# Optimization experiments

Hardware: AMD Instinct MI355X
Metric: run time of the kernel (lower is better)

Reference implementation:

```python
import jax, jax.numpy as jnp
import numpy as np

EPS = 1e-5  # torch LayerNorm default


def setup_inputs() -> dict:
    key = jax.random.key(0)
    ks = jax.random.split(key, 16)
    B, S, E = 2, 2048, 1024
    H, DK, DV = 16, 64, 64
    s_in = 1.0 / np.sqrt(E)
    s_ctx = 1.0 / np.sqrt(H * DV)
    return {
        "Q": jax.random.normal(ks[0], (B, S, E), jnp.float32),
        "K": jax.random.normal(ks[1], (B, S, E), jnp.float32),
        "V": jax.random.normal(ks[2], (B, S, E), jnp.float32),
        "attn_mask": jax.random.randint(ks[3], (B, S, S), 0, 2).astype(bool),
        "Wq": jax.random.normal(ks[4], (E, H * DK), jnp.float32) * s_in,
        "bq": jnp.zeros((H * DK,), jnp.float32),
        "Wk": jax.random.normal(ks[5], (E, H * DK), jnp.float32) * s_in,
        "bk": jnp.zeros((H * DK,), jnp.float32),
        "Wv": jax.random.normal(ks[6], (E, H * DV), jnp.float32) * s_in,
        "bv": jnp.zeros((H * DV,), jnp.float32),
        "Wo": jax.random.normal(ks[7], (H * DV, E), jnp.float32) * s_ctx,
        "bo": jnp.zeros((E,), jnp.float32),
        "gamma": jnp.ones((E,), jnp.float32),
        "beta": jnp.zeros((E,), jnp.float32),
        "n_heads": 16,
        "d_k": 64,
        "d_v": 64,
    }


def reference(Q, K, V, attn_mask, Wq, bq, Wk, bk, Wv, bv, Wo, bo, gamma, beta,
              n_heads, d_k, d_v):
    B, S, E = Q.shape
    # QKV projections -> [B, H, S, d]
    q = (Q @ Wq + bq).reshape(B, S, n_heads, d_k).transpose(0, 2, 1, 3)
    k = (K @ Wk + bk).reshape(B, S, n_heads, d_k).transpose(0, 2, 1, 3)
    v = (V @ Wv + bv).reshape(B, S, n_heads, d_v).transpose(0, 2, 1, 3)
    # scaled dot-product attention with explicit [B,H,S,S] scores
    scores = jnp.einsum('bhqd,bhkd->bhqk', q, k) / np.sqrt(d_k).astype(jnp.float32)
    scores = jnp.where(attn_mask[:, None, :, :], jnp.float32(-1e9), scores)
    attn = jax.nn.softmax(scores, axis=-1)
    context = jnp.einsum('bhqk,bhkd->bhqd', attn, v)
    context = context.transpose(0, 2, 1, 3).reshape(B, S, n_heads * d_v)
    output = context @ Wo + bo
    # residual + LayerNorm over last dim
    x = output + Q
    mu = jnp.mean(x, axis=-1, keepdims=True)
    var = jnp.mean(jnp.square(x - mu), axis=-1, keepdims=True)
    y = (x - mu) * jax.lax.rsqrt(var + EPS) * gamma + beta
    return (y, attn)
```

## Files before the change

### kernel.cpp

```cpp
#include <hip/hip_runtime.h>
#include <cstdint>
#include <cstddef>

#define Bc 2
#define Sc 2048
#define Ec 1024
#define Hc 16
#define Dc 64
#define BSc 4096
#define BHc 32

typedef __attribute__((ext_vector_type(8))) short bf16x8;
typedef __attribute__((ext_vector_type(4))) float f32x4;

__device__ __forceinline__ uint16_t f2b(float x) {
  union { float f; uint32_t u; } v; v.f = x;
  return (uint16_t)((v.u + 0x7FFFu + ((v.u >> 16) & 1u)) >> 16);
}

__device__ __forceinline__ uint4 pack8(const float* f) {
  union { uint16_t u[8]; uint4 v; } pk;
#pragma unroll
  for (int i = 0; i < 8; i++) pk.u[i] = f2b(f[i]);
  return pk.v;
}

__global__ void conv_bf16(const float* __restrict__ src, uint16_t* __restrict__ dst, int n) {
  int i = (blockIdx.x * blockDim.x + threadIdx.x) * 4;
  if (i < n) {
    float4 v = *(const float4*)(src + i);
    ushort4 o;
    o.x = f2b(v.x); o.y = f2b(v.y); o.z = f2b(v.z); o.w = f2b(v.w);
    *(ushort4*)(dst + i) = o;
  }
}

__global__ void transpose_bf16(const float* __restrict__ src, uint16_t* __restrict__ dst) {
  __shared__ uint16_t tile[32][33];
  int x0 = blockIdx.x * 32, y0 = blockIdx.y * 32;
  int tx = threadIdx.x & 31, ty = threadIdx.x >> 5;
#pragma unroll
  for (int i = 0; i < 32; i += 8)
    tile[ty + i][tx] = f2b(src[(size_t)(y0 + ty + i) * 1024 + x0 + tx]);
  __syncthreads();
#pragma unroll
  for (int i = 0; i < 32; i += 8)
    dst[(size_t)(x0 + ty + i) * 1024 + y0 + tx] = tile[tx][ty + i];
}

__global__ __launch_bounds__(256) void gemm_proj(
    const uint16_t* __restrict__ A, const uint16_t* __restrict__ BT,
    const float* __restrict__ bias, uint16_t* __restrict__ out, int mode) {
  const int K = 1024;
  __shared__ uint16_t As[128 * 40];
  __shared__ uint16_t Bs[128 * 40];
  int n0 = blockIdx.x * 128, m0 = blockIdx.y * 128;
  int t = threadIdx.x;
  int wave = t >> 6, lane = t & 63;
  int wm = (wave >> 1) * 64, wn = (wave & 1) * 64;
  int quad = lane >> 4, l16 = lane & 15;

  f32x4 acc[4][4];
#pragma unroll
  for (int i = 0; i < 4; i++)
#pragma unroll
    for (int j = 0; j < 4; j++) acc[i][j] = (f32x4)(0.0f);

  int srow = t >> 1, scol = (t & 1) * 16;

  for (int k0 = 0; k0 < K; k0 += 32) {
    const uint16_t* ag = A + (size_t)(m0 + srow) * K + k0 + scol;
    const uint16_t* bg = BT + (size_t)(n0 + srow) * K + k0 + scol;
    uint4 av0 = *(const uint4*)ag;
    uint4 av1 = *(const uint4*)(ag + 8);
    uint4 bv0 = *(const uint4*)bg;
    uint4 bv1 = *(const uint4*)(bg + 8);
    __syncthreads();
    *(uint4*)(As + srow * 40 + scol) = av0;
    *(uint4*)(As + srow * 40 + scol + 8) = av1;
    *(uint4*)(Bs + srow * 40 + scol) = bv0;
    *(uint4*)(Bs + srow * 40 + scol + 8) = bv1;
    __syncthreads();
    bf16x8 af[4], bfr[4];
#pragma unroll
    for (int i = 0; i < 4; i++)
      af[i] = *(const bf16x8*)(As + (wm + i * 16 + l16) * 40 + quad * 8);
#pragma unroll
    for (int j = 0; j < 4; j++)
      bfr[j] = *(const bf16x8*)(Bs + (wn + j * 16 + l16) * 40 + quad * 8);
#pragma unroll
    for (int i = 0; i < 4; i++)
#pragma unroll
      for (int j = 0; j < 4; j++)
        acc[i][j] = __builtin_amdgcn_mfma_f32_16x16x32_bf16(af[i], bfr[j], acc[i][j], 0, 0, 0);
  }
#pragma unroll
  for (int i = 0; i < 4; i++)
#pragma unroll
    for (int j = 0; j < 4; j++) {
      int col = n0 + wn + j * 16 + l16;
      float bval = bias[col];
      int h = col >> 6, d = col & 63;
#pragma unroll
      for (int r = 0; r < 4; r++) {
        int row = m0 + wm + i * 16 + quad * 4 + r;
        int b = row >> 11, s = row & 2047;
        uint16_t hv = f2b(acc[i][j][r] + bval);
        if (mode == 0)
          out[(size_t)((b * Hc + h) * Sc + s) * Dc + d] = hv;
        else
          out[(size_t)((b * Hc + h) * Dc + d) * Sc + s] = hv;
      }
    }
}

__global__ __launch_bounds__(256) void gemm_out(
    const uint16_t* __restrict__ A, const uint16_t* __restrict__ BT,
    const float* __restrict__ bias, const float* __restrict__ resid,
    float* __restrict__ x) {
  const int K = 1024;
  __shared__ uint16_t As[128 * 40];
  __shared__ uint16_t Bs[128 * 40];
  int n0 = blockIdx.x * 128, m0 = blockIdx.y * 128;
  int t = threadIdx.x;
  int wave = t >> 6, lane = t & 63;
  int wm = (wave >> 1) * 64, wn = (wave & 1) * 64;
  int quad = lane >> 4, l16 = lane & 15;

  f32x4 acc[4][4];
#pragma unroll
  for (int i = 0; i < 4; i++)
#pragma unroll
    for (int j = 0; j < 4; j++) acc[i][j] = (f32x4)(0.0f);

  int srow = t >> 1, scol = (t & 1) * 16;
  for (int k0 = 0; k0 < K; k0 += 32) {
    const uint16_t* ag = A + (size_t)(m0 + srow) * K + k0 + scol;
    const uint16_t* bg = BT + (size_t)(n0 + srow) * K + k0 + scol;
    uint4 av0 = *(const uint4*)ag;
    uint4 av1 = *(const uint4*)(ag + 8);
    uint4 bv0 = *(const uint4*)bg;
    uint4 bv1 = *(const uint4*)(bg + 8);
    __syncthreads();
    *(uint4*)(As + srow * 40 + scol) = av0;
    *(uint4*)(As + srow * 40 + scol + 8) = av1;
    *(uint4*)(Bs + srow * 40 + scol) = bv0;
    *(uint4*)(Bs + srow * 40 + scol + 8) = bv1;
    __syncthreads();
    bf16x8 af[4], bfr[4];
#pragma unroll
    for (int i = 0; i < 4; i++)
      af[i] = *(const bf16x8*)(As + (wm + i * 16 + l16) * 40 + quad * 8);
#pragma unroll
    for (int j = 0; j < 4; j++)
      bfr[j] = *(const bf16x8*)(Bs + (wn + j * 16 + l16) * 40 + quad * 8);
#pragma unroll
    for (int i = 0; i < 4; i++)
#pragma unroll
      for (int j = 0; j < 4; j++)
        acc[i][j] = __builtin_amdgcn_mfma_f32_16x16x32_bf16(af[i], bfr[j], acc[i][j], 0, 0, 0);
  }
#pragma unroll
  for (int i = 0; i < 4; i++)
#pragma unroll
    for (int j = 0; j < 4; j++) {
      int col = n0 + wn + j * 16 + l16;
      float bval = bias[col];
#pragma unroll
      for (int r = 0; r < 4; r++) {
        int row = m0 + wm + i * 16 + quad * 4 + r;
        x[(size_t)row * 1024 + col] = acc[i][j][r] + bval + resid[(size_t)row * 1024 + col];
      }
    }
}

__global__ __launch_bounds__(256) void scores_kernel(
    const uint16_t* __restrict__ q,
    const uint16_t* __restrict__ k,
    const int* __restrict__ mask,
    float* __restrict__ attn,
    float* __restrict__ rowsum) {
  __shared__ uint16_t Qs[128 * 72];
  __shared__ uint16_t Ks[128 * 72];
  int n0 = blockIdx.x * 128, m0 = blockIdx.y * 128;
  int bh = blockIdx.z;
  int b = bh >> 4;
  int t = threadIdx.x;
  int wave = t >> 6, lane = t & 63;
  int wm = (wave >> 1) * 64, wn = (wave & 1) * 64;
  int quad = lane >> 4, l16 = lane & 15;

  int srow = t >> 1, scol = (t & 1) * 32;
  {
    const uint16_t* qg = q + (size_t)(bh * Sc + m0 + srow) * Dc + scol;
    const uint16_t* kg = k + (size_t)(bh * Sc + n0 + srow) * Dc + scol;
#pragma unroll
    for (int c = 0; c < 4; c++)
      *(uint4*)(Qs + srow * 72 + scol + c * 8) = *(const uint4*)(qg + c * 8);
#pragma unroll
    for (int c = 0; c < 4; c++)
      *(uint4*)(Ks + srow * 72 + scol + c * 8) = *(const uint4*)(kg + c * 8);
  }
  __syncthreads();

  f32x4 acc[4][4];
#pragma unroll
  for (int i = 0; i < 4; i++)
#pragma unroll
    for (int j = 0; j < 4; j++) acc[i][j] = (f32x4)(0.0f);

#pragma unroll
  for (int kk = 0; kk < 2; kk++) {
    bf16x8 af[4], bfr[4];
#pragma unroll
    for (int i = 0; i < 4; i++)
      af[i] = *(const bf16x8*)(Qs + (wm + i * 16 + l16) * 72 + kk * 32 + quad * 8);
#pragma unroll
    for (int j = 0; j < 4; j++)
      bfr[j] = *(const bf16x8*)(Ks + (wn + j * 16 + l16) * 72 + kk * 32 + quad * 8);
#pragma unroll
    for (int i = 0; i < 4; i++)
#pragma unroll
      for (int j = 0; j < 4; j++)
        acc[i][j] = __builtin_amdgcn_mfma_f32_16x16x32_bf16(af[i], bfr[j], acc[i][j], 0, 0, 0);
  }

#pragma unroll
  for (int i = 0; i < 4; i++) {
#pragma unroll
    for (int r = 0; r < 4; r++) {
      int m = m0 + wm + i * 16 + quad * 4 + r;
      const int* mrow = mask + (size_t)(b * Sc + m) * Sc;
      float* arow = attn + ((size_t)(bh * Sc + m)) * Sc;
      float rs = 0.0f;
#pragma unroll
      for (int j = 0; j < 4; j++) {
        int n = n0 + wn + j * 16 + l16;
        float sc = acc[i][j][r] * 0.125f;
        float p = mrow[n] ? 0.0f : __expf(sc);
        arow[n] = p;
        rs += p;
      }
      rs += __shfl_xor(rs, 1);
      rs += __shfl_xor(rs, 2);
      rs += __shfl_xor(rs, 4);
      rs += __shfl_xor(rs, 8);
      if (l16 == 0) atomicAdd(&rowsum[bh * Sc + m], rs);
    }
  }
}

__global__ void inv_kernel(const float* __restrict__ rowsum, float* __restrict__ rowinv, int n) {
  int i = blockIdx.x * blockDim.x + threadIdx.x;
  if (i < n) rowinv[i] = 1.0f / rowsum[i];
}

__global__ __launch_bounds__(256) void context_kernel(
    float* __restrict__ attn,
    const float* __restrict__ rowinv,
    const uint16_t* __restrict__ vT,
    uint16_t* __restrict__ ctx) {
  __shared__ uint16_t As[64 * 72];
  __shared__ uint16_t Vs[64 * 72];
  int m0 = blockIdx.x * 64;
  int bh = blockIdx.y;
  int t = threadIdx.x;
  int wave = t >> 6, lane = t & 63;
  int quad = lane >> 4, l16 = lane & 15;

  f32x4 acc[4];
#pragma unroll
  for (int j = 0; j < 4; j++) acc[j] = (f32x4)(0.0f);

  int arow = t >> 2, acol = (t & 3) * 16;
  float inv_r = rowinv[bh * Sc + m0 + arow];
  int vrow = t >> 2, vcol = (t & 3) * 16;

  for (int k0 = 0; k0 < Sc; k0 += 64) {
    float* ag = attn + ((size_t)(bh * Sc + m0 + arow)) * Sc + k0 + acol;
    float va[16];
    float4 a0 = *(const float4*)ag;
    float4 a1 = *(const float4*)(ag + 4);
    float4 a2 = *(const float4*)(ag + 8);
    float4 a3 = *(const float4*)(ag + 12);
    va[0] = a0.x * inv_r;  va[1] = a0.y * inv_r;  va[2] = a0.z * inv_r;  va[3] = a0.w * inv_r;
    va[4] = a1.x * inv_r;  va[5] = a1.y * inv_r;  va[6] = a1.z * inv_r;  va[7] = a1.w * inv_r;
    va[8] = a2.x * inv_r;  va[9] = a2.y * inv_r;  va[10] = a2.z * inv_r; va[11] = a2.w * inv_r;
    va[12] = a3.x * inv_r; va[13] = a3.y * inv_r; va[14] = a3.z * inv_r; va[15] = a3.w * inv_r;
    float4 w0 = make_float4(va[0], va[1], va[2], va[3]);
    float4 w1 = make_float4(va[4], va[5], va[6], va[7]);
    float4 w2 = make_float4(va[8], va[9], va[10], va[11]);
    float4 w3 = make_float4(va[12], va[13], va[14], va[15]);
    *(float4*)ag = w0;
    *(float4*)(ag + 4) = w1;
    *(float4*)(ag + 8) = w2;
    *(float4*)(ag + 12) = w3;
    const uint16_t* vg = vT + ((size_t)(bh * Dc + vrow)) * Sc + k0 + vcol;
    uint4 vv0 = *(const uint4*)vg;
    uint4 vv1 = *(const uint4*)(vg + 8);
    __syncthreads();
    *(uint4*)(As + arow * 72 + acol) = pack8(va);
    *(uint4*)(As + arow * 72 + acol + 8) = pack8(va + 8);
    *(uint4*)(Vs + vrow * 72 + vcol) = vv0;
    *(uint4*)(Vs + vrow * 72 + vcol + 8) = vv1;
    __syncthreads();
#pragma unroll
    for (int kk = 0; kk < 2; kk++) {
      bf16x8 af = *(const bf16x8*)(As + (wave * 16 + l16) * 72 + kk * 32 + quad * 8);
#pragma unroll
      for (int j = 0; j < 4; j++) {
        bf16x8 bfr = *(const bf16x8*)(Vs + (j * 16 + l16) * 72 + kk * 32 + quad * 8);
        acc[j] = __builtin_amdgcn_mfma_f32_16x16x32_bf16(af, bfr, acc[j], 0, 0, 0);
      }
    }
    __syncthreads();
  }
  int b = bh >> 4, h = bh & 15;
#pragma unroll
  for (int j = 0; j < 4; j++) {
    int d = j * 16 + l16;
#pragma unroll
    for (int r = 0; r < 4; r++) {
      int s = m0 + wave * 16 + quad * 4 + r;
      ctx[(size_t)(b * Sc + s) * (Hc * Dc) + h * Dc + d] = f2b(acc[j][r]);
    }
  }
}

__global__ __launch_bounds__(256) void ln_kernel(
    const float* __restrict__ x, const float* __restrict__ gamma,
    const float* __restrict__ beta, float* __restrict__ y) {
  int row = blockIdx.x;
  int t = threadIdx.x;
  const float* xr = x + (size_t)row * 1024;
  float4 v = *(const float4*)(xr + t * 4);
  float s = v.x + v.y + v.z + v.w;
  float s2 = v.x * v.x + v.y * v.y + v.z * v.z + v.w * v.w;
#pragma unroll
  for (int o = 1; o < 64; o <<= 1) {
    s += __shfl_xor(s, o);
    s2 += __shfl_xor(s2, o);
  }
  __shared__ float ss[4], ss2[4];
  int wave = t >> 6, lane = t & 63;
  if (lane == 0) { ss[wave] = s; ss2[wave] = s2; }
  __syncthreads();
  s = ss[0] + ss[1] + ss[2] + ss[3];
  s2 = ss2[0] + ss2[1] + ss2[2] + ss2[3];
  float mu = s * (1.0f / 1024.0f);
  float var = s2 * (1.0f / 1024.0f) - mu * mu;
  float rstd = rsqrtf(var + 1e-5f);
  float4 g = *(const float4*)(gamma + t * 4);
  float4 be = *(const float4*)(beta + t * 4);
  float4 o;
  o.x = (v.x - mu) * rstd * g.x + be.x;
  o.y = (v.y - mu) * rstd * g.y + be.y;
  o.z = (v.z - mu) * rstd * g.z + be.z;
  o.w = (v.w - mu) * rstd * g.w + be.w;
  *(float4*)(y + (size_t)row * 1024 + t * 4) = o;
}

extern "C" void kernel_launch(void* const* d_in, const int* in_sizes, int n_in,
                              void* d_out, int out_size, void* d_ws, size_t ws_size,
                              hipStream_t stream) {
  const float* Q = (const float*)d_in[0];
  const float* K = (const float*)d_in[1];
  const float* V = (const float*)d_in[2];
  const int* mask = (const int*)d_in[3];
  const float* Wq = (const float*)d_in[4];
  const float* bq = (const float*)d_in[5];
  const float* Wk = (const float*)d_in[6];
  const float* bk = (const float*)d_in[7];
  const float* Wv = (const float*)d_in[8];
  const float* bv = (const float*)d_in[9];
  const float* Wo = (const float*)d_in[10];
  const float* bo = (const float*)d_in[11];
  const float* gamma = (const float*)d_in[12];
  const float* beta = (const float*)d_in[13];

  float* y = (float*)d_out;
  float* attn = (float*)d_out + (size_t)BSc * Ec;

  char* ws = (char*)d_ws;
  size_t off = 0;
  auto alloc = [&](size_t bytes) -> void* {
    void* p = ws + off;
    off = (off + bytes + 255) & ~(size_t)255;
    return p;
  };
  uint16_t* Qb  = (uint16_t*)alloc((size_t)BSc * Ec * 2);
  uint16_t* Kb  = (uint16_t*)alloc((size_t)BSc * Ec * 2);
  uint16_t* Vb  = (uint16_t*)alloc((size_t)BSc * Ec * 2);
  uint16_t* WqT = (uint16_t*)alloc((size_t)Ec * Ec * 2);
  uint16_t* WkT = (uint16_t*)alloc((size_t)Ec * Ec * 2);
  uint16_t* WvT = (uint16_t*)alloc((size_t)Ec * Ec * 2);
  uint16_t* WoT = (uint16_t*)alloc((size_t)Ec * Ec * 2);
  uint16_t* qh  = (uint16_t*)alloc((size_t)BHc * Sc * Dc * 2);
  uint16_t* kh  = (uint16_t*)alloc((size_t)BHc * Sc * Dc * 2);
  uint16_t* vT  = (uint16_t*)alloc((size_t)BHc * Dc * Sc * 2);
  uint16_t* ctx = (uint16_t*)alloc((size_t)BSc * Ec * 2);
  float* xres   = (float*)alloc((size_t)BSc * Ec * 4);
  float* rowsum = (float*)alloc((size_t)BHc * Sc * 4);
  float* rowinv = (float*)alloc((size_t)BHc * Sc * 4);

  const int n_qkv = BSc * Ec;

  conv_bf16<<<n_qkv / 1024, 256, 0, stream>>>(Q, Qb, n_qkv);
  conv_bf16<<<n_qkv / 1024, 256, 0, stream>>>(K, Kb, n_qkv);
  conv_bf16<<<n_qkv / 1024, 256, 0, stream>>>(V, Vb, n_qkv);
  dim3 tg(32, 32);
  transpose_bf16<<<tg, 256, 0, stream>>>(Wq, WqT);
  transpose_bf16<<<tg, 256, 0, stream>>>(Wk, WkT);
  transpose_bf16<<<tg, 256, 0, stream>>>(Wv, WvT);
  transpose_bf16<<<tg, 256, 0, stream>>>(Wo, WoT);
  dim3 pg(Ec / 128, BSc / 128);
  gemm_proj<<<pg, 256, 0, stream>>>(Qb, WqT, bq, qh, 0);
  gemm_proj<<<pg, 256, 0, stream>>>(Kb, WkT, bk, kh, 0);
  gemm_proj<<<pg, 256, 0, stream>>>(Vb, WvT, bv, vT, 1);
  hipMemsetAsync(rowsum, 0, (size_t)BHc * Sc * 4, stream);
  dim3 sg(Sc / 128, Sc / 128, BHc);
  scores_kernel<<<sg, 256, 0, stream>>>(qh, kh, mask, attn, rowsum);
  inv_kernel<<<(BHc * Sc) / 256, 256, 0, stream>>>(rowsum, rowinv, BHc * Sc);
  dim3 cg(Sc / 64, BHc);
  context_kernel<<<cg, 256, 0, stream>>>(attn, rowinv, vT, ctx);
  gemm_out<<<pg, 256, 0, stream>>>(ctx, WoT, bo, Q, xres);
  ln_kernel<<<BSc, 256, 0, stream>>>(xres, gamma, beta, y);
}
```

Baseline: 1.116 ms.

## Fuse scores, softmax normalization and context into a two-pass attention kernel

Replaces the separate scores, inverse-rowsum and context kernels with a single kernel per 64-row query tile. A first pass computes QK^T and masked exp only to accumulate row sums in registers. A second pass recomputes the scores, writes the normalized attention once, and feeds bf16 probabilities through shared memory into the PV MFMA. This removes the unnormalized attn write plus the read-modify-write of the 512MB attention matrix, the atomics, the memset and the extra launches. In exchange QK^T and the mask are computed and read twice.

After: 1.022 ms. -8.4%, faster.

```diff
diff --git a/kernel.cpp b/kernel.cpp
--- a/kernel.cpp
+++ b/kernel.cpp
@@ -16,13 +16,6 @@
 __device__ __forceinline__ uint16_t f2b(float x) {
   union { float f; uint32_t u; } v; v.f = x;
   return (uint16_t)((v.u + 0x7FFFu + ((v.u >> 16) & 1u)) >> 16);
-}
-
-__device__ __forceinline__ uint4 pack8(const float* f) {
-  union { uint16_t u[8]; uint4 v; } pk;
-#pragma unroll
-  for (int i = 0; i < 8; i++) pk.u[i] = f2b(f[i]);
-  return pk.v;
 }
 
 __global__ void conv_bf16(const float* __restrict__ src, uint16_t* __restrict__ dst, int n) {
@@ -174,155 +167,141 @@
     }
 }
 
-__global__ __launch_bounds__(256) void scores_kernel(
-    const uint16_t* __restrict__ q,
-    const uint16_t* __restrict__ k,
+__global__ __launch_bounds__(256) void fused_attn(
+    const uint16_t* __restrict__ qh,
+    const uint16_t* __restrict__ kh,
+    const uint16_t* __restrict__ vT,
     const int* __restrict__ mask,
     float* __restrict__ attn,
-    float* __restrict__ rowsum) {
-  __shared__ uint16_t Qs[128 * 72];
-  __shared__ uint16_t Ks[128 * 72];
-  int n0 = blockIdx.x * 128, m0 = blockIdx.y * 128;
-  int bh = blockIdx.z;
+    uint16_t* __restrict__ ctx) {
+  __shared__ uint16_t Qs[64 * 72];
+  __shared__ uint16_t Ks[64 * 72];
+  __shared__ uint16_t Vs[64 * 72];
+  __shared__ uint16_t Ps[64 * 72];
+  __shared__ float rinv_s[64];
+
+  int m0 = blockIdx.x * 64;
+  int bh = blockIdx.y;
   int b = bh >> 4;
   int t = threadIdx.x;
   int wave = t >> 6, lane = t & 63;
-  int wm = (wave >> 1) * 64, wn = (wave & 1) * 64;
   int quad = lane >> 4, l16 = lane & 15;
 
-  int srow = t >> 1, scol = (t & 1) * 32;
+  int srow = t >> 2, scol = (t & 3) * 16;
+
   {
-    const uint16_t* qg = q + (size_t)(bh * Sc + m0 + srow) * Dc + scol;
-    const uint16_t* kg = k + (size_t)(bh * Sc + n0 + srow) * Dc + scol;
-#pragma unroll
-    for (int c = 0; c < 4; c++)
-      *(uint4*)(Qs + srow * 72 + scol + c * 8) = *(const uint4*)(qg + c * 8);
-#pragma unroll
-    for (int c = 0; c < 4; c++)
-      *(uint4*)(Ks + srow * 72 + scol + c * 8) = *(const uint4*)(kg + c * 8);
+    const uint16_t* qg = qh + (size_t)(bh * Sc + m0 + srow) * Dc + scol;
+    uint4 q0 = *(const uint4*)qg;
+    uint4 q1 = *(const uint4*)(qg + 8);
+    *(uint4*)(Qs + srow * 72 + scol) = q0;
+    *(uint4*)(Qs + srow * 72 + scol + 8) = q1;
   }
   __syncthreads();
 
-  f32x4 acc[4][4];
-#pragma unroll
-  for (int i = 0; i < 4; i++)
-#pragma unroll
-    for (int j = 0; j < 4; j++) acc[i][j] = (f32x4)(0.0f);
-
-#pragma unroll
-  for (int kk = 0; kk < 2; kk++) {
-    bf16x8 af[4], bfr[4];
-#pragma unroll
-    for (int i = 0; i < 4; i++)
-      af[i] = *(const bf16x8*)(Qs + (wm + i * 16 + l16) * 72 + kk * 32 + quad * 8);
+  int m = m0 + wave * 16 + l16;
+  const int* mrow = mask + (size_t)(b * Sc + m) * Sc;
+
+  bf16x8 qf0 = *(const bf16x8*)(Qs + (wave * 16 + l16) * 72 + quad * 8);
+  bf16x8 qf1 = *(const bf16x8*)(Qs + (wave * 16 + l16) * 72 + 32 + quad * 8);
+
+  float rs = 0.0f;
+  for (int k0 = 0; k0 < Sc; k0 += 64) {
+    const uint16_t* kg = kh + (size_t)(bh * Sc + k0 + srow) * Dc + scol;
+    uint4 kv0 = *(const uint4*)kg;
+    uint4 kv1 = *(const uint4*)(kg + 8);
+    __syncthreads();
+    *(uint4*)(Ks + srow * 72 + scol) = kv0;
+    *(uint4*)(Ks + srow * 72 + scol + 8) = kv1;
+    __syncthreads();
+    int4 mv[4];
 #pragma unroll
     for (int j = 0; j < 4; j++)
-      bfr[j] = *(const bf16x8*)(Ks + (wn + j * 16 + l16) * 72 + kk * 32 + quad * 8);
-#pragma unroll
-    for (int i = 0; i < 4; i++)
-#pragma unroll
-      for (int j = 0; j < 4; j++)
-        acc[i][j] = __builtin_amdgcn_mfma_f32_16x16x32_bf16(af[i], bfr[j], acc[i][j], 0, 0, 0);
-  }
-
-#pragma unroll
-  for (int i = 0; i < 4; i++) {
-#pragma unroll
-    for (int r = 0; r < 4; r++) {
-      int m = m0 + wm + i * 16 + quad * 4 + r;
-      const int* mrow = mask + (size_t)(b * Sc + m) * Sc;
-      float* arow = attn + ((size_t)(bh * Sc + m)) * Sc;
-      float rs = 0.0f;
-#pragma unroll
-      for (int j = 0; j < 4; j++) {
-        int n = n0 + wn + j * 16 + l16;
-        float sc = acc[i][j][r] * 0.125f;
-        float p = mrow[n] ? 0.0f : __expf(sc);
-        arow[n] = p;
-        rs += p;
-      }
-      rs += __shfl_xor(rs, 1);
-      rs += __shfl_xor(rs, 2);
-      rs += __shfl_xor(rs, 4);
-      rs += __shfl_xor(rs, 8);
-      if (l16 == 0) atomicAdd(&rowsum[bh * Sc + m], rs);
-    }
-  }
-}
-
-__global__ void inv_kernel(const float* __restrict__ rowsum, float* __restrict__ rowinv, int n) {
-  int i = blockIdx.x * blockDim.x + threadIdx.x;
-  if (i < n) rowinv[i] = 1.0f / rowsum[i];
-}
-
-__global__ __launch_bounds__(256) void context_kernel(
-    float* __restrict__ attn,
-    const float* __restrict__ rowinv,
-    const uint16_t* __restrict__ vT,
-    uint16_t* __restrict__ ctx) {
-  __shared__ uint16_t As[64 * 72];
-  __shared__ uint16_t Vs[64 * 72];
-  int m0 = blockIdx.x * 64;
-  int bh = blockIdx.y;
-  int t = threadIdx.x;
-  int wave = t >> 6, lane = t & 63;
-  int quad = lane >> 4, l16 = lane & 15;
-
-  f32x4 acc[4];
-#pragma unroll
-  for (int j = 0; j < 4; j++) acc[j] = (f32x4)(0.0f);
-
-  int arow = t >> 2, acol = (t & 3) * 16;
-  float inv_r = rowinv[bh * Sc + m0 + arow];
-  int vrow = t >> 2, vcol = (t & 3) * 16;
+      mv[j] = *(const int4*)(mrow + k0 + j * 16 + quad * 4);
+    f32x4 sacc[4];
+#pragma unroll
+    for (int j = 0; j < 4; j++) sacc[j] = (f32x4)(0.0f);
+#pragma unroll
+    for (int j = 0; j < 4; j++) {
+      bf16x8 kf0 = *(const bf16x8*)(Ks + (j * 16 + l16) * 72 + quad * 8);
+      bf16x8 kf1 = *(const bf16x8*)(Ks + (j * 16 + l16) * 72 + 32 + quad * 8);
+      sacc[j] = __builtin_amdgcn_mfma_f32_16x16x32_bf16(kf0, qf0, sacc[j], 0, 0, 0);
+      sacc[j] = __builtin_amdgcn_mfma_f32_16x16x32_bf16(kf1, qf1, sacc[j], 0, 0, 0);
+    }
+#pragma unroll
+    for (int j = 0; j < 4; j++) {
+      rs += mv[j].x ? 0.0f : __expf(sacc[j][0] * 0.125f);
+      rs += mv[j].y ? 0.0f : __expf(sacc[j][1] * 0.125f);
+      rs += mv[j].z ? 0.0f : __expf(sacc[j][2] * 0.125f);
+      rs += mv[j].w ? 0.0f : __expf(sacc[j][3] * 0.125f);
+    }
+  }
+  rs += __shfl_xor(rs, 16);
+  rs += __shfl_xor(rs, 32);
+  if (lane < 16) rinv_s[wave * 16 + l16] = 1.0f / rs;
+  __syncthreads();
+  float rv = rinv_s[wave * 16 + l16];
+
+  f32x4 cacc[4];
+#pragma unroll
+  for (int j = 0; j < 4; j++) cacc[j] = (f32x4)(0.0f);
 
   for (int k0 = 0; k0 < Sc; k0 += 64) {
-    float* ag = attn + ((size_t)(bh * Sc + m0 + arow)) * Sc + k0 + acol;
-    float va[16];
-    float4 a0 = *(const float4*)ag;
-    float4 a1 = *(const float4*)(ag + 4);
-    float4 a2 = *(const float4*)(ag + 8);
-    float4 a3 = *(const float4*)(ag + 12);
-    va[0] = a0.x * inv_r;  va[1] = a0.y * inv_r;  va[2] = a0.z * inv_r;  va[3] = a0.w * inv_r;
-    va[4] = a1.x * inv_r;  va[5] = a1.y * inv_r;  va[6] = a1.z * inv_r;  va[7] = a1.w * inv_r;
-    va[8] = a2.x * inv_r;  va[9] = a2.y * inv_r;  va[10] = a2.z * inv_r; va[11] = a2.w * inv_r;
-    va[12] = a3.x * inv_r; va[13] = a3.y * inv_r; va[14] = a3.z * inv_r; va[15] = a3.w * inv_r;
-    float4 w0 = make_float4(va[0], va[1], va[2], va[3]);
-    float4 w1 = make_float4(va[4], va[5], va[6], va[7]);
-    float4 w2 = make_float4(va[8], va[9], va[10], va[11]);
-    float4 w3 = make_float4(va[12], va[13], va[14], va[15]);
-    *(float4*)ag = w0;
-    *(float4*)(ag + 4) = w1;
-    *(float4*)(ag + 8) = w2;
-    *(float4*)(ag + 12) = w3;
-    const uint16_t* vg = vT + ((size_t)(bh * Dc + vrow)) * Sc + k0 + vcol;
+    const uint16_t* kg = kh + (size_t)(bh * Sc + k0 + srow) * Dc + scol;
+    const uint16_t* vg = vT + (size_t)(bh * Dc + srow) * Sc + k0 + scol;
+    uint4 kv0 = *(const uint4*)kg;
+    uint4 kv1 = *(const uint4*)(kg + 8);
     uint4 vv0 = *(const uint4*)vg;
     uint4 vv1 = *(const uint4*)(vg + 8);
     __syncthreads();
-    *(uint4*)(As + arow * 72 + acol) = pack8(va);
-    *(uint4*)(As + arow * 72 + acol + 8) = pack8(va + 8);
-    *(uint4*)(Vs + vrow * 72 + vcol) = vv0;
-    *(uint4*)(Vs + vrow * 72 + vcol + 8) = vv1;
-    __syncthreads();
-#pragma unroll
-    for (int kk = 0; kk < 2; kk++) {
-      bf16x8 af = *(const bf16x8*)(As + (wave * 16 + l16) * 72 + kk * 32 + quad * 8);
-#pragma unroll
-      for (int j = 0; j < 4; j++) {
-        bf16x8 bfr = *(const bf16x8*)(Vs + (j * 16 + l16) * 72 + kk * 32 + quad * 8);
-        acc[j] = __builtin_amdgcn_mfma_f32_16x16x32_bf16(af, bfr, acc[j], 0, 0, 0);
-      }
-    }
-    __syncthreads();
-  }
-  int b = bh >> 4, h = bh & 15;
+    *(uint4*)(Ks + srow * 72 + scol) = kv0;
+    *(uint4*)(Ks + srow * 72 + scol + 8) = kv1;
+    *(uint4*)(Vs + srow * 72 + scol) = vv0;
+    *(uint4*)(Vs + srow * 72 + scol + 8) = vv1;
+    __syncthreads();
+    int4 mv[4];
+#pragma unroll
+    for (int j = 0; j < 4; j++)
+      mv[j] = *(const int4*)(mrow + k0 + j * 16 + quad * 4);
+    f32x4 sacc[4];
+#pragma unroll
+    for (int j = 0; j < 4; j++) sacc[j] = (f32x4)(0.0f);
+#pragma unroll
+    for (int j = 0; j < 4; j++) {
+      bf16x8 kf0 = *(const bf16x8*)(Ks + (j * 16 + l16) * 72 + quad * 8);
+      bf16x8 kf1 = *(const bf16x8*)(Ks + (j * 16 + l16) * 72 + 32 + quad * 8);
+      sacc[j] = __builtin_amdgcn_mfma_f32_16x16x32_bf16(kf0, qf0, sacc[j], 0, 0, 0);
+      sacc[j] = __builtin_amdgcn_mfma_f32_16x16x32_bf16(kf1, qf1, sacc[j], 0, 0, 0);
+    }
+    float* arow = attn + (size_t)(bh * Sc + m) * Sc + k0;
+#pragma unroll
+    for (int j = 0; j < 4; j++) {
+      float p0 = mv[j].x ? 0.0f : __expf(sacc[j][0] * 0.125f) * rv;
+      float p1 = mv[j].y ? 0.0f : __expf(sacc[j][1] * 0.125f) * rv;
+      float p2 = mv[j].z ? 0.0f : __expf(sacc[j][2] * 0.125f) * rv;
+      float p3 = mv[j].w ? 0.0f : __expf(sacc[j][3] * 0.125f) * rv;
+      *(float4*)(arow + j * 16 + quad * 4) = make_float4(p0, p1, p2, p3);
+      union { uint16_t u[4]; uint2 v; } pk;
+      pk.u[0] = f2b(p0); pk.u[1] = f2b(p1); pk.u[2] = f2b(p2); pk.u[3] = f2b(p3);
+      *(uint2*)(Ps + (wave * 16 + l16) * 72 + j * 16 + quad * 4) = pk.v;
+    }
+    bf16x8 pf0 = *(const bf16x8*)(Ps + (wave * 16 + l16) * 72 + quad * 8);
+    bf16x8 pf1 = *(const bf16x8*)(Ps + (wave * 16 + l16) * 72 + 32 + quad * 8);
+#pragma unroll
+    for (int j = 0; j < 4; j++) {
+      bf16x8 vf0 = *(const bf16x8*)(Vs + (j * 16 + l16) * 72 + quad * 8);
+      bf16x8 vf1 = *(const bf16x8*)(Vs + (j * 16 + l16) * 72 + 32 + quad * 8);
+      cacc[j] = __builtin_amdgcn_mfma_f32_16x16x32_bf16(pf0, vf0, cacc[j], 0, 0, 0);
+      cacc[j] = __builtin_amdgcn_mfma_f32_16x16x32_bf16(pf1, vf1, cacc[j], 0, 0, 0);
+    }
+  }
+  int h = bh & 15;
 #pragma unroll
   for (int j = 0; j < 4; j++) {
     int d = j * 16 + l16;
 #pragma unroll
     for (int r = 0; r < 4; r++) {
       int s = m0 + wave * 16 + quad * 4 + r;
-      ctx[(size_t)(b * Sc + s) * (Hc * Dc) + h * Dc + d] = f2b(acc[j][r]);
+      ctx[(size_t)(b * Sc + s) * (Hc * Dc) + h * Dc + d] = f2b(cacc[j][r]);
     }
   }
 }
@@ -400,8 +379,6 @@
   uint16_t* vT  = (uint16_t*)alloc((size_t)BHc * Dc * Sc * 2);
   uint16_t* ctx = (uint16_t*)alloc((size_t)BSc * Ec * 2);
   float* xres   = (float*)alloc((size_t)BSc * Ec * 4);
-  float* rowsum = (float*)alloc((size_t)BHc * Sc * 4);
-  float* rowinv = (float*)alloc((size_t)BHc * Sc * 4);
 
   const int n_qkv = BSc * Ec;
 
@@ -417,12 +394,8 @@
   gemm_proj<<<pg, 256, 0, stream>>>(Qb, WqT, bq, qh, 0);
   gemm_proj<<<pg, 256, 0, stream>>>(Kb, WkT, bk, kh, 0);
   gemm_proj<<<pg, 256, 0, stream>>>(Vb, WvT, bv, vT, 1);
-  hipMemsetAsync(rowsum, 0, (size_t)BHc * Sc * 4, stream);
-  dim3 sg(Sc / 128, Sc / 128, BHc);
-  scores_kernel<<<sg, 256, 0, stream>>>(qh, kh, mask, attn, rowsum);
-  inv_kernel<<<(BHc * Sc) / 256, 256, 0, stream>>>(rowsum, rowinv, BHc * Sc);
-  dim3 cg(Sc / 64, BHc);
-  context_kernel<<<cg, 256, 0, stream>>>(attn, rowinv, vT, ctx);
+  dim3 fg(Sc / 64, BHc);
+  fused_attn<<<fg, 256, 0, stream>>>(qh, kh, vT, mask, attn, ctx);
   gemm_out<<<pg, 256, 0, stream>>>(ctx, WoT, bo, Q, xres);
   ln_kernel<<<BSc, 256, 0, stream>>>(xres, gamma, beta, y);
 }
```
